# Optimization experiments

Measured on AMD Instinct MI355X. Metric: run time of the kernel, lower is better.

The kernel has to match this reference:

```python
import jax, jax.numpy as jnp
import numpy as np

D_MODEL = 1024
HEADS = 16


def setup_inputs() -> dict:
    key = jax.random.key(0)
    ks = jax.random.split(key, 6)
    B, N, d = 4, 1024, D_MODEL
    s = 1.0 / np.sqrt(d)
    return {
        "x": jax.random.normal(ks[0], (B, N, d), dtype=jnp.float32),
        "attn_bias": jax.random.normal(ks[1], (B, HEADS, N, N), dtype=jnp.float32),
        "Wq": jax.random.normal(ks[2], (d, d), dtype=jnp.float32) * s,
        "Wk": jax.random.normal(ks[3], (d, d), dtype=jnp.float32) * s,
        "Wv": jax.random.normal(ks[4], (d, d), dtype=jnp.float32) * s,
        "Wo": jax.random.normal(ks[5], (d, d), dtype=jnp.float32) * s,
    }


def reference(x, attn_bias, Wq, Wk, Wv, Wo):
    B, N, d = x.shape
    H = HEADS
    hd = d // H
    # projections -> [B, H, N, hd] (torch Linear: x @ W.T)
    q = (x @ Wq.T).reshape(B, N, H, hd).transpose(0, 2, 1, 3)
    k = (x @ Wk.T).reshape(B, N, H, hd).transpose(0, 2, 1, 3)
    v = (x @ Wv.T).reshape(B, N, H, hd).transpose(0, 2, 1, 3)
    scale = hd ** -0.5
    attn = jnp.einsum('bhqd,bhkd->bhqk', q, k) * scale + attn_bias
    attn = jax.nn.softmax(attn, axis=-1)
    out = jnp.einsum('bhqk,bhkd->bhqd', attn, v)
    out = out.transpose(0, 2, 1, 3).reshape(B, N, d)
    return out @ Wo.T
```

## Files before the change

kernel.cpp:

```cpp
#include <hip/hip_runtime.h>
#include <hip/hip_bf16.h>
#include <math.h>


typedef __bf16 bf16;
typedef bf16 bf16x8 __attribute__((ext_vector_type(8)));
typedef bf16 bf16x4 __attribute__((ext_vector_type(4)));
typedef float floatx4 __attribute__((ext_vector_type(4)));

#define MFMA16(a, b, c) __builtin_amdgcn_mfma_f32_16x16x32_bf16((a), (b), (c), 0, 0, 0)

__device__ __forceinline__ void gload_lds16(const bf16* g, bf16* l) {
  __builtin_amdgcn_global_load_lds(
      (const __attribute__((address_space(1))) unsigned int*)g,
      (__attribute__((address_space(3))) unsigned int*)l, 16, 0, 0);
}

__global__ __launch_bounds__(256) void cvt_kernel(
    const float* __restrict__ x, const float* __restrict__ wq,
    const float* __restrict__ wk, const float* __restrict__ wv,
    const float* __restrict__ wo, bf16* __restrict__ dst) {
  long e = ((long)blockIdx.x * 256 + threadIdx.x) * 4;
  const float* src;
  if (e < 4194304) {
    src = x + e;
  } else {
    long r = (e - 4194304) >> 20;
    long off = (e - 4194304) & 1048575;
    src = (r == 0 ? wq : r == 1 ? wk : r == 2 ? wv : wo) + off;
  }
  float4 v = *reinterpret_cast<const float4*>(src);
  bf16x4 o = { (bf16)v.x, (bf16)v.y, (bf16)v.z, (bf16)v.w };
  *reinterpret_cast<bf16x4*>(dst + e) = o;
}

__device__ __forceinline__ void gemm_mainloop(const bf16* __restrict__ Ag,
                                              const bf16* __restrict__ Bg,
                                              bf16* As, bf16* Bs,
                                              floatx4 acc[4][4]) {
  int tid = threadIdx.x;
  int w = tid >> 6, l = tid & 63, g = l >> 4, ln = l & 15;
  int wr = (w >> 1) << 6, wc = (w & 1) << 6;
  int lrow = w * 16 + (l >> 2);
  int lkc = (l & 3) * 8;
  for (int k0 = 0; k0 < 1024; k0 += 32) {
    __syncthreads();
    gload_lds16(Ag + (size_t)lrow * 1024 + k0 + lkc, As + w * 512);
    gload_lds16(Ag + (size_t)(lrow + 64) * 1024 + k0 + lkc, As + 2048 + w * 512);
    gload_lds16(Bg + (size_t)lrow * 1024 + k0 + lkc, Bs + w * 512);
    gload_lds16(Bg + (size_t)(lrow + 64) * 1024 + k0 + lkc, Bs + 2048 + w * 512);
    asm volatile("s_waitcnt vmcnt(0)" ::: "memory");
    __syncthreads();
    bf16x8 af[4], bfv[4];
#pragma unroll
    for (int t = 0; t < 4; t++) {
      af[t] = *(const bf16x8*)&As[(wr + t * 16 + ln) * 32 + g * 8];
      bfv[t] = *(const bf16x8*)&Bs[(wc + t * 16 + ln) * 32 + g * 8];
    }
#pragma unroll
    for (int i = 0; i < 4; i++)
#pragma unroll
      for (int j = 0; j < 4; j++)
        acc[i][j] = MFMA16(af[i], bfv[j], acc[i][j]);
  }
}

__global__ __launch_bounds__(256) void qkv_proj(
    const bf16* __restrict__ xb, const bf16* __restrict__ wqkv,
    bf16* __restrict__ Qo, bf16* __restrict__ Ko, bf16* __restrict__ Vo) {
  __shared__ bf16 As[4096], Bs[4096];
  const floatx4 z4 = {0.f, 0.f, 0.f, 0.f};
  floatx4 acc[4][4];
#pragma unroll
  for (int i = 0; i < 4; i++)
#pragma unroll
    for (int j = 0; j < 4; j++) acc[i][j] = z4;
  int z = blockIdx.z;
  const bf16* Ag = xb + (size_t)blockIdx.x * 128 * 1024;
  const bf16* Bg = wqkv + (size_t)z * 1048576 + (size_t)blockIdx.y * 128 * 1024;
  gemm_mainloop(Ag, Bg, As, Bs, acc);
  bf16* dst = z == 0 ? Qo : (z == 1 ? Ko : Vo);
  int tid = threadIdx.x, w = tid >> 6, l = tid & 63, g = l >> 4, ln = l & 15;
  int mbase = blockIdx.x * 128 + ((w >> 1) << 6);
  int ibase = blockIdx.y * 128 + ((w & 1) << 6);
#pragma unroll
  for (int i = 0; i < 4; i++)
#pragma unroll
    for (int j = 0; j < 4; j++)
#pragma unroll
      for (int r = 0; r < 4; r++) {
        int m = mbase + i * 16 + g * 4 + r;
        int col = ibase + j * 16 + ln;
        int b = m >> 10, n = m & 1023, h = col >> 6, di = col & 63;
        dst[((size_t)((b * 16 + h) * 1024 + n) << 6) + di] = (bf16)acc[i][j][r];
      }
}

__global__ __launch_bounds__(256) void flash_kernel(
    const bf16* __restrict__ Q, const bf16* __restrict__ Kg,
    const bf16* __restrict__ Vg, const float* __restrict__ bias,
    bf16* __restrict__ Ao) {
  __shared__ bf16 Klds[2][64 * 72];
  __shared__ bf16 Vtlds[2][64 * 72];
  __shared__ bf16 Plds[4 * 16 * 72];
  int tid = threadIdx.x;
  int w = tid >> 6, l = tid & 63, g = l >> 4, ln = l & 15;
  int qt = blockIdx.x;
  int bh = blockIdx.y;
  size_t bhN = (size_t)bh * 1024;

  int skey = l, skc2 = w * 2;
  const bf16* Kbase = Kg + (bhN + skey) * 64;
  const bf16* Vbase = Vg + (bhN + skey) * 64;

  bf16x8 kr[2], vr[2];
#pragma unroll
  for (int c = 0; c < 2; c++) {
    kr[c] = *(const bf16x8*)(Kbase + (skc2 + c) * 8);
    vr[c] = *(const bf16x8*)(Vbase + (skc2 + c) * 8);
  }

  const bf16* qptr = Q + (bhN + qt * 64 + w * 16 + ln) * 64;
  bf16x8 qf0 = *(const bf16x8*)(qptr + g * 8);
  bf16x8 qf1 = *(const bf16x8*)(qptr + 32 + g * 8);

  const float* bbase = bias + ((bhN + qt * 64 + w * 16 + g * 4) << 10) + ln;
  float bc[4][4];
#pragma unroll
  for (int t = 0; t < 4; t++)
#pragma unroll
    for (int r = 0; r < 4; r++) bc[t][r] = bbase[(size_t)r * 1024 + t * 16];

  const floatx4 z4 = {0.f, 0.f, 0.f, 0.f};
  floatx4 o[4];
  float m_i[4], l_i[4];
#pragma unroll
  for (int i = 0; i < 4; i++) { o[i] = z4; m_i[i] = -1e30f; l_i[i] = 0.f; }

#pragma unroll
  for (int c = 0; c < 2; c++) {
    int kc = skc2 + c;
    *(bf16x8*)&Klds[0][skey * 72 + kc * 8] = kr[c];
#pragma unroll
    for (int j = 0; j < 8; j++) Vtlds[0][(kc * 8 + j) * 72 + skey] = vr[c][j];
  }
  __syncthreads();

  bf16* pw = Plds + w * 16 * 72;

#pragma unroll 2
  for (int kb = 0; kb < 16; kb++) {
    int cur = kb & 1, nxt = cur ^ 1;
    float bn[4][4];
    if (kb < 15) {
#pragma unroll
      for (int c = 0; c < 2; c++) {
        kr[c] = *(const bf16x8*)(Kbase + (kb + 1) * 4096 + (skc2 + c) * 8);
        vr[c] = *(const bf16x8*)(Vbase + (kb + 1) * 4096 + (skc2 + c) * 8);
      }
      const float* bp = bbase + (kb + 1) * 64;
#pragma unroll
      for (int t = 0; t < 4; t++)
#pragma unroll
        for (int r = 0; r < 4; r++) bn[t][r] = bp[(size_t)r * 1024 + t * 16];
    }

    floatx4 s[4];
#pragma unroll
    for (int t = 0; t < 4; t++) {
      s[t] = z4;
      bf16x8 kf0 = *(const bf16x8*)&Klds[cur][(t * 16 + ln) * 72 + g * 8];
      bf16x8 kf1 = *(const bf16x8*)&Klds[cur][(t * 16 + ln) * 72 + 32 + g * 8];
      s[t] = MFMA16(qf0, kf0, s[t]);
      s[t] = MFMA16(qf1, kf1, s[t]);
    }
#pragma unroll
    for (int t = 0; t < 4; t++)
#pragma unroll
      for (int r = 0; r < 4; r++)
        s[t][r] = fmaf(s[t][r], 0.125f, bc[t][r]);

    float cmax[4], rs[4], alpha[4];
#pragma unroll
    for (int r = 0; r < 4; r++)
      cmax[r] = fmaxf(fmaxf(s[0][r], s[1][r]), fmaxf(s[2][r], s[3][r]));
#pragma unroll
    for (int mk = 1; mk < 16; mk <<= 1)
#pragma unroll
      for (int r = 0; r < 4; r++)
        cmax[r] = fmaxf(cmax[r], __shfl_xor(cmax[r], mk, 64));
#pragma unroll
    for (int r = 0; r < 4; r++) {
      float mn = fmaxf(m_i[r], cmax[r]);
      alpha[r] = __expf(m_i[r] - mn);
      m_i[r] = mn;
      rs[r] = 0.f;
    }
#pragma unroll
    for (int t = 0; t < 4; t++)
#pragma unroll
      for (int r = 0; r < 4; r++) {
        float p = __expf(s[t][r] - m_i[r]);
        s[t][r] = p;
        rs[r] += p;
      }
#pragma unroll
    for (int mk = 1; mk < 16; mk <<= 1)
#pragma unroll
      for (int r = 0; r < 4; r++) rs[r] += __shfl_xor(rs[r], mk, 64);
#pragma unroll
    for (int r = 0; r < 4; r++) l_i[r] = l_i[r] * alpha[r] + rs[r];
#pragma unroll
    for (int dt = 0; dt < 4; dt++)
#pragma unroll
      for (int r = 0; r < 4; r++) o[dt][r] *= alpha[r];

#pragma unroll
    for (int t = 0; t < 4; t++)
#pragma unroll
      for (int r = 0; r < 4; r++)
        pw[(g * 4 + r) * 72 + t * 16 + ln] = (bf16)s[t][r];
    asm volatile("s_waitcnt lgkmcnt(0)" ::: "memory");

    bf16x8 pf0 = *(const bf16x8*)&pw[ln * 72 + g * 8];
    bf16x8 pf1 = *(const bf16x8*)&pw[ln * 72 + 32 + g * 8];
#pragma unroll
    for (int dt = 0; dt < 4; dt++) {
      bf16x8 vf0 = *(const bf16x8*)&Vtlds[cur][(dt * 16 + ln) * 72 + g * 8];
      bf16x8 vf1 = *(const bf16x8*)&Vtlds[cur][(dt * 16 + ln) * 72 + 32 + g * 8];
      o[dt] = MFMA16(pf0, vf0, o[dt]);
      o[dt] = MFMA16(pf1, vf1, o[dt]);
    }

    if (kb < 15) {
#pragma unroll
      for (int c = 0; c < 2; c++) {
        int kc = skc2 + c;
        *(bf16x8*)&Klds[nxt][skey * 72 + kc * 8] = kr[c];
#pragma unroll
        for (int j = 0; j < 8; j++)
          Vtlds[nxt][(kc * 8 + j) * 72 + skey] = vr[c][j];
      }
#pragma unroll
      for (int t = 0; t < 4; t++)
#pragma unroll
        for (int r = 0; r < 4; r++) bc[t][r] = bn[t][r];
      __syncthreads();
    }
  }

  int b = bh >> 4, h = bh & 15;
#pragma unroll
  for (int r = 0; r < 4; r++) {
    float inv = 1.f / l_i[r];
    int row = b * 1024 + qt * 64 + w * 16 + g * 4 + r;
    bf16* op = Ao + (size_t)row * 1024 + h * 64 + ln;
#pragma unroll
    for (int dt = 0; dt < 4; dt++) op[dt * 16] = (bf16)(o[dt][r] * inv);
  }
}

__global__ __launch_bounds__(256) void out_proj(const bf16* __restrict__ Ab,
                                                const bf16* __restrict__ wob,
                                                float* __restrict__ C) {
  __shared__ bf16 As[4096], Bs[2048];
  const floatx4 z4 = {0.f, 0.f, 0.f, 0.f};
  floatx4 acc[4][2];
#pragma unroll
  for (int i = 0; i < 4; i++)
#pragma unroll
    for (int j = 0; j < 2; j++) acc[i][j] = z4;
  const bf16* Ag = Ab + (size_t)blockIdx.x * 128 * 1024;
  const bf16* Bg = wob + (size_t)blockIdx.y * 64 * 1024;
  int tid = threadIdx.x;
  int w = tid >> 6, l = tid & 63, g = l >> 4, ln = l & 15;
  int wr = (w >> 1) << 6, wc = (w & 1) << 5;
  int lrow = w * 16 + (l >> 2);
  int lkc = (l & 3) * 8;
  for (int k0 = 0; k0 < 1024; k0 += 32) {
    __syncthreads();
    gload_lds16(Ag + (size_t)lrow * 1024 + k0 + lkc, As + w * 512);
    gload_lds16(Ag + (size_t)(lrow + 64) * 1024 + k0 + lkc, As + 2048 + w * 512);
    gload_lds16(Bg + (size_t)lrow * 1024 + k0 + lkc, Bs + w * 512);
    asm volatile("s_waitcnt vmcnt(0)" ::: "memory");
    __syncthreads();
    bf16x8 af[4], bfv[2];
#pragma unroll
    for (int t = 0; t < 4; t++)
      af[t] = *(const bf16x8*)&As[(wr + t * 16 + ln) * 32 + g * 8];
#pragma unroll
    for (int t = 0; t < 2; t++)
      bfv[t] = *(const bf16x8*)&Bs[(wc + t * 16 + ln) * 32 + g * 8];
#pragma unroll
    for (int i = 0; i < 4; i++)
#pragma unroll
      for (int j = 0; j < 2; j++)
        acc[i][j] = MFMA16(af[i], bfv[j], acc[i][j]);
  }
  int mbase = blockIdx.x * 128 + wr;
  int cbase = blockIdx.y * 64 + wc;
#pragma unroll
  for (int i = 0; i < 4; i++)
#pragma unroll
    for (int j = 0; j < 2; j++)
#pragma unroll
      for (int r = 0; r < 4; r++)
        C[(size_t)(mbase + i * 16 + g * 4 + r) * 1024 + cbase + j * 16 + ln] =
            acc[i][j][r];
}

extern "C" void kernel_launch(void* const* d_in, const int* in_sizes, int n_in,
                              void* d_out, int out_size, void* d_ws, size_t ws_size,
                              hipStream_t stream) {
  const float* x = (const float*)d_in[0];
  const float* bias = (const float*)d_in[1];
  const float* Wq = (const float*)d_in[2];
  const float* Wk = (const float*)d_in[3];
  const float* Wv = (const float*)d_in[4];
  const float* Wo = (const float*)d_in[5];
  float* out = (float*)d_out;

  bf16* xb = (bf16*)d_ws;
  bf16* wqkv = xb + 4194304;
  bf16* wob = wqkv + 3 * 1048576;
  bf16* Qb = wob + 1048576;
  bf16* Kb = Qb + 4194304;
  bf16* Vb = Kb + 4194304;
  bf16* Ao = Vb + 4194304;

  cvt_kernel<<<8192, 256, 0, stream>>>(x, Wq, Wk, Wv, Wo, xb);
  qkv_proj<<<dim3(32, 8, 3), 256, 0, stream>>>(xb, wqkv, Qb, Kb, Vb);
  flash_kernel<<<dim3(16, 64), 256, 0, stream>>>(Qb, Kb, Vb, bias, Ao);
  out_proj<<<dim3(32, 16), 256, 0, stream>>>(Ao, wob, out);
}
```

Measured before the change: 459.2 us.

## Pre-transpose V and stream K/V into swizzled LDS via direct global-to-LDS loads

Adds a separate kernel that transposes V into a per-head [hd, N] layout, so the flash kernel no longer does scalar per-element transposing stores into LDS. K and V^T tiles are then loaded straight into LDS with global_load_lds, using an XOR-swizzled unpadded layout to avoid bank conflicts. This frees registers and removes the staging through VGPRs. The block index is also remapped to change scheduling order across heads. The cost is an extra kernel launch and an extra round trip of V through global memory.

```diff
diff --git a/kernel.cpp b/kernel.cpp
--- a/kernel.cpp
+++ b/kernel.cpp
@@ -96,29 +96,56 @@
       }
 }
 
+__global__ __launch_bounds__(256) void vtrans(const bf16* __restrict__ V,
+                                              bf16* __restrict__ Vt) {
+  __shared__ __align__(16) bf16 t[64][72];
+  int bh = blockIdx.y, nb = blockIdx.x;
+  const bf16* src = V + ((size_t)bh * 1024 + nb * 64) * 64;
+  int tid = threadIdx.x;
+  int r = tid >> 2, c = (tid & 3) * 16;
+  bf16x8 a = *(const bf16x8*)(src + (size_t)r * 64 + c);
+  bf16x8 b = *(const bf16x8*)(src + (size_t)r * 64 + c + 8);
+  *(bf16x8*)&t[r][c] = a;
+  *(bf16x8*)&t[r][c + 8] = b;
+  __syncthreads();
+  bf16* dst = Vt + ((size_t)bh * 64 + r) * 1024 + nb * 64 + c;
+  bf16x8 o0, o1;
+#pragma unroll
+  for (int j = 0; j < 8; j++) o0[j] = t[c + j][r];
+#pragma unroll
+  for (int j = 0; j < 8; j++) o1[j] = t[c + 8 + j][r];
+  *(bf16x8*)dst = o0;
+  *(bf16x8*)(dst + 8) = o1;
+}
+
 __global__ __launch_bounds__(256) void flash_kernel(
     const bf16* __restrict__ Q, const bf16* __restrict__ Kg,
-    const bf16* __restrict__ Vg, const float* __restrict__ bias,
+    const bf16* __restrict__ Vt, const float* __restrict__ bias,
     bf16* __restrict__ Ao) {
-  __shared__ bf16 Klds[2][64 * 72];
-  __shared__ bf16 Vtlds[2][64 * 72];
-  __shared__ bf16 Plds[4 * 16 * 72];
+  __shared__ __align__(16) bf16 Klds[2][4096];
+  __shared__ __align__(16) bf16 Vlds[2][4096];
+  __shared__ __align__(16) bf16 Plds[4 * 16 * 72];
   int tid = threadIdx.x;
   int w = tid >> 6, l = tid & 63, g = l >> 4, ln = l & 15;
-  int qt = blockIdx.x;
-  int bh = blockIdx.y;
+  int flat = blockIdx.y * 16 + blockIdx.x;
+  int lg = (flat & 7) * 128 + (flat >> 3);
+  int qt = lg & 15;
+  int bh = lg >> 4;
   size_t bhN = (size_t)bh * 1024;
 
-  int skey = l, skc2 = w * 2;
-  const bf16* Kbase = Kg + (bhN + skey) * 64;
-  const bf16* Vbase = Vg + (bhN + skey) * 64;
-
-  bf16x8 kr[2], vr[2];
-#pragma unroll
-  for (int c = 0; c < 2; c++) {
-    kr[c] = *(const bf16x8*)(Kbase + (skc2 + c) * 8);
-    vr[c] = *(const bf16x8*)(Vbase + (skc2 + c) * 8);
-  }
+  int D0 = w * 2048 + l * 16;
+  int D1 = D0 + 1024;
+  int S0 = D0 ^ (((D0 >> 7) & 7) << 4);
+  int S1 = D1 ^ (((D1 >> 7) & 7) << 4);
+  const bf16* Ks0 = Kg + bhN * 64 + (S0 >> 1);
+  const bf16* Ks1 = Kg + bhN * 64 + (S1 >> 1);
+  const bf16* Vs0 = Vt + bhN * 64 + (size_t)(S0 >> 7) * 1024 + ((S0 & 127) >> 1);
+  const bf16* Vs1 = Vt + bhN * 64 + (size_t)(S1 >> 7) * 1024 + ((S1 & 127) >> 1);
+
+  gload_lds16(Ks0, &Klds[0][w * 1024]);
+  gload_lds16(Ks1, &Klds[0][w * 1024 + 512]);
+  gload_lds16(Vs0, &Vlds[0][w * 1024]);
+  gload_lds16(Vs1, &Vlds[0][w * 1024 + 512]);
 
   const bf16* qptr = Q + (bhN + qt * 64 + w * 16 + ln) * 64;
   bf16x8 qf0 = *(const bf16x8*)(qptr + g * 8);
@@ -137,13 +164,11 @@
 #pragma unroll
   for (int i = 0; i < 4; i++) { o[i] = z4; m_i[i] = -1e30f; l_i[i] = 0.f; }
 
-#pragma unroll
-  for (int c = 0; c < 2; c++) {
-    int kc = skc2 + c;
-    *(bf16x8*)&Klds[0][skey * 72 + kc * 8] = kr[c];
-#pragma unroll
-    for (int j = 0; j < 8; j++) Vtlds[0][(kc * 8 + j) * 72 + skey] = vr[c][j];
-  }
+  int sx = (ln & 7) << 4;
+  int rc0 = (g * 16) ^ sx;
+  int rc1 = (64 + g * 16) ^ sx;
+
+  asm volatile("s_waitcnt vmcnt(0)" ::: "memory");
   __syncthreads();
 
   bf16* pw = Plds + w * 16 * 72;
@@ -153,11 +178,10 @@
     int cur = kb & 1, nxt = cur ^ 1;
     float bn[4][4];
     if (kb < 15) {
-#pragma unroll
-      for (int c = 0; c < 2; c++) {
-        kr[c] = *(const bf16x8*)(Kbase + (kb + 1) * 4096 + (skc2 + c) * 8);
-        vr[c] = *(const bf16x8*)(Vbase + (kb + 1) * 4096 + (skc2 + c) * 8);
-      }
+      gload_lds16(Ks0 + (kb + 1) * 4096, &Klds[nxt][w * 1024]);
+      gload_lds16(Ks1 + (kb + 1) * 4096, &Klds[nxt][w * 1024 + 512]);
+      gload_lds16(Vs0 + (kb + 1) * 64, &Vlds[nxt][w * 1024]);
+      gload_lds16(Vs1 + (kb + 1) * 64, &Vlds[nxt][w * 1024 + 512]);
       const float* bp = bbase + (kb + 1) * 64;
 #pragma unroll
       for (int t = 0; t < 4; t++)
@@ -165,12 +189,13 @@
         for (int r = 0; r < 4; r++) bn[t][r] = bp[(size_t)r * 1024 + t * 16];
     }
 
+    const char* Kc = (const char*)&Klds[cur][0];
     floatx4 s[4];
 #pragma unroll
     for (int t = 0; t < 4; t++) {
       s[t] = z4;
-      bf16x8 kf0 = *(const bf16x8*)&Klds[cur][(t * 16 + ln) * 72 + g * 8];
-      bf16x8 kf1 = *(const bf16x8*)&Klds[cur][(t * 16 + ln) * 72 + 32 + g * 8];
+      bf16x8 kf0 = *(const bf16x8*)(Kc + (t * 16 + ln) * 128 + rc0);
+      bf16x8 kf1 = *(const bf16x8*)(Kc + (t * 16 + ln) * 128 + rc1);
       s[t] = MFMA16(qf0, kf0, s[t]);
       s[t] = MFMA16(qf1, kf1, s[t]);
     }
@@ -224,27 +249,21 @@
 
     bf16x8 pf0 = *(const bf16x8*)&pw[ln * 72 + g * 8];
     bf16x8 pf1 = *(const bf16x8*)&pw[ln * 72 + 32 + g * 8];
+    const char* Vc = (const char*)&Vlds[cur][0];
 #pragma unroll
     for (int dt = 0; dt < 4; dt++) {
-      bf16x8 vf0 = *(const bf16x8*)&Vtlds[cur][(dt * 16 + ln) * 72 + g * 8];
-      bf16x8 vf1 = *(const bf16x8*)&Vtlds[cur][(dt * 16 + ln) * 72 + 32 + g * 8];
+      bf16x8 vf0 = *(const bf16x8*)(Vc + (dt * 16 + ln) * 128 + rc0);
+      bf16x8 vf1 = *(const bf16x8*)(Vc + (dt * 16 + ln) * 128 + rc1);
       o[dt] = MFMA16(pf0, vf0, o[dt]);
       o[dt] = MFMA16(pf1, vf1, o[dt]);
     }
 
     if (kb < 15) {
 #pragma unroll
-      for (int c = 0; c < 2; c++) {
-        int kc = skc2 + c;
-        *(bf16x8*)&Klds[nxt][skey * 72 + kc * 8] = kr[c];
-#pragma unroll
-        for (int j = 0; j < 8; j++)
-          Vtlds[nxt][(kc * 8 + j) * 72 + skey] = vr[c][j];
-      }
-#pragma unroll
       for (int t = 0; t < 4; t++)
 #pragma unroll
         for (int r = 0; r < 4; r++) bc[t][r] = bn[t][r];
+      asm volatile("s_waitcnt vmcnt(0)" ::: "memory");
       __syncthreads();
     }
   }
@@ -327,9 +346,11 @@
   bf16* Kb = Qb + 4194304;
   bf16* Vb = Kb + 4194304;
   bf16* Ao = Vb + 4194304;
+  bf16* Vtb = Ao + 4194304;
 
   cvt_kernel<<<8192, 256, 0, stream>>>(x, Wq, Wk, Wv, Wo, xb);
   qkv_proj<<<dim3(32, 8, 3), 256, 0, stream>>>(xb, wqkv, Qb, Kb, Vb);
-  flash_kernel<<<dim3(16, 64), 256, 0, stream>>>(Qb, Kb, Vb, bias, Ao);
+  vtrans<<<dim3(16, 64), 256, 0, stream>>>(Vb, Vtb);
+  flash_kernel<<<dim3(16, 64), 256, 0, stream>>>(Qb, Kb, Vtb, bias, Ao);
   out_proj<<<dim3(32, 16), 256, 0, stream>>>(Ao, wob, out);
 }
```

Result: slower. 476.0 us (+3.6%).
